# Kernel tuning notes

Measured on AMD Instinct MI355X. Metric: run time of the kernel, lower is better.

## Reference

```python
import jax, jax.numpy as jnp
import numpy as np

N = 100000
E = 1600000
D_IN = 128
D_HID = 128
D_OUT = 16


def setup_inputs() -> dict:
    key = jax.random.key(0)
    ks = jax.random.split(key, 10)
    x = jax.random.normal(ks[0], (N, D_IN), dtype=jnp.float32)
    edge_index = jax.random.randint(ks[1], (2, E), 0, N, dtype=jnp.int32)
    s = 1.0 / np.sqrt(D_IN)
    sh = 1.0 / np.sqrt(D_HID)
    W1l = jax.random.uniform(ks[2], (D_HID, D_IN), jnp.float32, -s, s)
    b1l = jax.random.uniform(ks[3], (D_HID,), jnp.float32, -s, s)
    W1r = jax.random.uniform(ks[4], (D_HID, D_IN), jnp.float32, -s, s)
    W2l = jax.random.uniform(ks[5], (D_HID, D_HID), jnp.float32, -sh, sh)
    b2l = jax.random.uniform(ks[6], (D_HID,), jnp.float32, -sh, sh)
    W2r = jax.random.uniform(ks[7], (D_HID, D_HID), jnp.float32, -sh, sh)
    Wc = jax.random.uniform(ks[8], (D_OUT, D_HID), jnp.float32, -sh, sh)
    bc = jax.random.uniform(ks[9], (D_OUT,), jnp.float32, -sh, sh)
    return {"x": x, "edge_index": edge_index, "W1l": W1l, "b1l": b1l, "W1r": W1r,
            "W2l": W2l, "b2l": b2l, "W2r": W2r, "Wc": Wc, "bc": bc}


def _sage_conv(x, src, dst, Wl, bl, Wr):
    # PyG SAGEConv (mean aggr): out_i = Wl @ mean_{j in N(i)} x_j + bl + Wr @ x_i
    n = x.shape[0]
    msg = x[src]                                             # [E, d] gather
    summed = jax.ops.segment_sum(msg, dst, num_segments=n)   # [N, d] scatter-add
    cnt = jax.ops.segment_sum(jnp.ones((src.shape[0],), x.dtype), dst, num_segments=n)
    agg = summed / jnp.maximum(cnt, 1.0)[:, None]            # mean; isolated nodes -> 0
    return agg @ Wl.T + bl + x @ Wr.T


def reference(x, edge_index, W1l, b1l, W1r, W2l, b2l, W2r, Wc, bc):
    src, dst = edge_index[0], edge_index[1]
    h = jax.nn.relu(_sage_conv(x, src, dst, W1l, b1l, W1r))
    # dropout p=0.5 is identity at inference (training=False)
    z = _sage_conv(h, src, dst, W2l, b2l, W2r)
    return z @ Wc.T + bc
```

## Files before the change

kernel.cpp:

```cpp
#include <hip/hip_runtime.h>

#define BSHIFT 9
#define BCAP   13312
#define CHUNK  8192

typedef __bf16 bf16x8 __attribute__((ext_vector_type(8)));
typedef float  f32x4  __attribute__((ext_vector_type(4)));
typedef float  f32x2  __attribute__((ext_vector_type(2)));

__device__ __forceinline__ unsigned short f2b(float f) {
  unsigned u = __float_as_uint(f);
  return (unsigned short)((u + 0x7fffu + ((u >> 16) & 1u)) >> 16);
}
__device__ __forceinline__ float b2f_lo(unsigned u) {
  return __uint_as_float(u << 16);
}
__device__ __forceinline__ float b2f_hi(unsigned u) {
  return __uint_as_float(u & 0xffff0000u);
}

__global__ __launch_bounds__(256) void k_front(
    const int* __restrict__ ei, int E, int* __restrict__ bcnt,
    unsigned* __restrict__ edg,
    const float* __restrict__ x, unsigned short* __restrict__ xb,
    unsigned* __restrict__ xq, int ngroups,
    const float* __restrict__ W1l, const float* __restrict__ W1r,
    unsigned short* __restrict__ Wb,
    const float* __restrict__ Wc, const float* __restrict__ bc,
    const float* __restrict__ W2l, const float* __restrict__ W2r,
    const float* __restrict__ b2, unsigned short* __restrict__ Mb,
    float* __restrict__ bias2,
    unsigned short* __restrict__ Pnb, int ZR, int nbin, int ncast) {
  __shared__ int lh[256], lbase[256], lcur[256];
  __shared__ int ldst[CHUNK];
  const int b = blockIdx.x;
  const int t = threadIdx.x;
  if (b < nbin) {
    lh[t] = 0; lcur[t] = 0;
    __syncthreads();
    const int e0 = b * CHUNK;
    const int n = min(E - e0, CHUNK);
    const int* __restrict__ src = ei;
    const int* __restrict__ dst = ei + E;
    for (int j = t; j < n; j += 256) {
      int d = dst[e0 + j];
      ldst[j] = d;
      atomicAdd(&lh[((unsigned)d) >> BSHIFT], 1);
    }
    __syncthreads();
    if (lh[t]) lbase[t] = atomicAdd(&bcnt[t], lh[t]);
    __syncthreads();
    for (int j = t; j < n; j += 256) {
      int d = ldst[j];
      unsigned s = (unsigned)src[e0 + j];
      int bk = ((unsigned)d) >> BSHIFT;
      int p = lbase[bk] + atomicAdd(&lcur[bk], 1);
      if (p < BCAP) edg[(size_t)bk * BCAP + p] = ((unsigned)(d & 511) << 17) | s;
    }
  } else if (b < nbin + ncast) {
    int g = (b - nbin) * 256 + t;
    if (g < ngroups) {
      float4 v = ((const float4*)x)[g];
      ushort4 o;
      o.x = f2b(v.x); o.y = f2b(v.y); o.z = f2b(v.z); o.w = f2b(v.w);
      ((ushort4*)xb)[g] = o;
      int q8 = __builtin_amdgcn_cvt_pk_fp8_f32(v.x, v.y, 0, false);
      q8 = __builtin_amdgcn_cvt_pk_fp8_f32(v.z, v.w, q8, true);
      xq[g] = (unsigned)q8;
    }
  } else {
    int bb = b - nbin - ncast;
    if (bb < 128) {
      int idx = bb * 256 + t;
      int col = idx >> 8, k = idx & 255;
      float v = (k < 128) ? W1l[col * 128 + k] : W1r[col * 128 + (k - 128)];
      Wb[col * 256 + k] = f2b(v);
    } else if (bb < 144) {
      int mb = bb - 128;
      int mat = mb >> 3;
      const float* W2 = mat ? W2r : W2l;
      int o = (mb & 7) * 2 + (t >> 7);
      int k = t & 127;
      float s = 0.f;
      for (int j = 0; j < 128; ++j) s = fmaf(Wc[o * 128 + j], W2[j * 128 + k], s);
      Mb[(size_t)(mat * 16 + o) * 128 + k] = f2b(s);
      if (mb == 0 && t < 16) {
        float sb = bc[t];
        for (int j = 0; j < 128; ++j) sb = fmaf(Wc[t * 128 + j], b2[j], sb);
        bias2[t] = sb;
      }
    } else {
      if (t < 64) ((unsigned*)(xb + (size_t)ZR * 128))[t] = 0;
      if (t < 32) xq[(size_t)ZR * 32 + t] = 0;
      if (t < 8)  ((unsigned*)(Pnb + (size_t)ZR * 16))[t] = 0;
    }
  }
}

__global__ __launch_bounds__(256) void k_build(
    const unsigned* __restrict__ edg, const int* __restrict__ bcnt,
    int* __restrict__ eidx, int* __restrict__ rowstart, int* __restrict__ cnt,
    int N, int ZR) {
  __shared__ int lsrc[BCAP];
  __shared__ int lcnt[512], lstart[512], lcur[512];
  __shared__ int wsum[4];
  const int b = blockIdx.x;
  const int t = threadIdx.x;
  const int node0 = b << BSHIFT;
  const int nb = min(512, N - node0);
  const int ecount = min(bcnt[b], BCAP);
  const unsigned* __restrict__ ed = edg + (size_t)b * BCAP;
  lcnt[2 * t] = 0; lcnt[2 * t + 1] = 0;
  for (int j = t; j < BCAP; j += 256) lsrc[j] = ZR;
  __syncthreads();
  for (int j = t; j < ecount; j += 256)
    atomicAdd(&lcnt[ed[j] >> 17], 1);
  __syncthreads();
  {
    int a0 = lcnt[2 * t], a1 = lcnt[2 * t + 1];
    int p0 = (a0 + 15) & ~15, p1 = (a1 + 15) & ~15;
    int s = p0 + p1, incl = s;
    int lane = t & 63, wv = t >> 6;
#pragma unroll
    for (int off = 1; off < 64; off <<= 1) {
      int v = __shfl_up(incl, off, 64);
      if (lane >= off) incl += v;
    }
    if (lane == 63) wsum[wv] = incl;
    __syncthreads();
    int woff = 0;
    for (int i = 0; i < wv; ++i) woff += wsum[i];
    int excl = woff + incl - s;
    lstart[2 * t] = excl;          lcur[2 * t] = excl;
    lstart[2 * t + 1] = excl + p0; lcur[2 * t + 1] = excl + p0;
  }
  __syncthreads();
  for (int j = t; j < ecount; j += 256) {
    unsigned e = ed[j];
    int p = atomicAdd(&lcur[e >> 17], 1);
    lsrc[p] = (int)(e & 0x1FFFFu);
  }
  __syncthreads();
  const int ebase = b * BCAP;
  int ecountp = min(wsum[0] + wsum[1] + wsum[2] + wsum[3], BCAP);
  for (int j = t; j < ecountp; j += 256) eidx[ebase + j] = lsrc[j];
  for (int i = t; i < nb; i += 256) {
    rowstart[node0 + i] = ebase + lstart[i];
    cnt[node0 + i] = lcnt[i];
  }
}

__global__ __launch_bounds__(256) void k_agg1(
    const int* __restrict__ eidx, const int* __restrict__ rowstart,
    const int* __restrict__ cnt,
    const unsigned* __restrict__ xq, unsigned short* __restrict__ aggb, int N) {
  int w = (blockIdx.x * 256 + threadIdx.x) >> 6;
  int lane = threadIdx.x & 63;
  if (w >= N) return;
  const int sub = lane >> 4;
  const int li = lane & 15;
  int deg = cnt[w];
  const int* el = eidx + rowstart[w];
  f32x2 acc[4];
#pragma unroll
  for (int j = 0; j < 4; ++j) acc[j] = (f32x2){0.f, 0.f};

  for (int e = 0; e < deg; e += 16) {
    int4 q = *(const int4*)(el + e + sub * 4);
    uint2 v0 = *(const uint2*)(xq + (size_t)q.x * 32 + li * 2);
    uint2 v1 = *(const uint2*)(xq + (size_t)q.y * 32 + li * 2);
    uint2 v2 = *(const uint2*)(xq + (size_t)q.z * 32 + li * 2);
    uint2 v3 = *(const uint2*)(xq + (size_t)q.w * 32 + li * 2);
#define ADD8(v)                                                      \
    acc[0] += __builtin_amdgcn_cvt_pk_f32_fp8(v.x, false);           \
    acc[1] += __builtin_amdgcn_cvt_pk_f32_fp8(v.x, true);            \
    acc[2] += __builtin_amdgcn_cvt_pk_f32_fp8(v.y, false);           \
    acc[3] += __builtin_amdgcn_cvt_pk_f32_fp8(v.y, true);
    ADD8(v0) ADD8(v1) ADD8(v2) ADD8(v3)
#undef ADD8
  }
#pragma unroll
  for (int j = 0; j < 4; ++j) {
    acc[j].x += __shfl_xor(acc[j].x, 16, 64);
    acc[j].y += __shfl_xor(acc[j].y, 16, 64);
    acc[j].x += __shfl_xor(acc[j].x, 32, 64);
    acc[j].y += __shfl_xor(acc[j].y, 32, 64);
  }
  if (sub == 0) {
    float sc = 1.0f / (float)max(deg, 1);
    uint2 o;
    uint4 o4;
    o4.x = (unsigned)f2b(acc[0].x * sc) | ((unsigned)f2b(acc[0].y * sc) << 16);
    o4.y = (unsigned)f2b(acc[1].x * sc) | ((unsigned)f2b(acc[1].y * sc) << 16);
    o4.z = (unsigned)f2b(acc[2].x * sc) | ((unsigned)f2b(acc[2].y * sc) << 16);
    o4.w = (unsigned)f2b(acc[3].x * sc) | ((unsigned)f2b(acc[3].y * sc) << 16);
    *(uint4*)(aggb + (size_t)w * 128 + li * 8) = o4;
    (void)o;
  }
}

__global__ __launch_bounds__(256) void k_gemm1_mfma(
    const unsigned short* __restrict__ aggb, const unsigned short* __restrict__ xb,
    const unsigned short* __restrict__ Wb, const float* __restrict__ b1,
    const unsigned short* __restrict__ Mb,
    unsigned short* __restrict__ Pnb, float* __restrict__ Ps, int N) {
  __shared__ union {
    struct { unsigned short A[128 * 40]; unsigned short W[128 * 40]; } s;
    unsigned short H[128 * 136];
  } sm;
  const int t = threadIdx.x;
  const int w = t >> 6;
  const int lane = t & 63;
  const int q = lane >> 4;
  const int l16 = lane & 15;
  const int row0 = blockIdx.x * 128;

  f32x4 acc[2][8];
#pragma unroll
  for (int rt = 0; rt < 2; ++rt)
#pragma unroll
    for (int ct = 0; ct < 8; ++ct) acc[rt][ct] = (f32x4){0.f, 0.f, 0.f, 0.f};

  for (int kc = 0; kc < 8; ++kc) {
    const unsigned short* Asrc = (kc < 4) ? aggb : xb;
    const int koff = (kc & 3) * 32;
#pragma unroll
    for (int i = 0; i < 2; ++i) {
      int idx = t + i * 256;
      int row = idx >> 2, c4 = idx & 3;
      int gr = row0 + row; if (gr >= N) gr = N - 1;
      uint4 v = *(const uint4*)(Asrc + (size_t)gr * 128 + koff + c4 * 8);
      *(uint4*)(sm.s.A + row * 40 + c4 * 8) = v;
    }
#pragma unroll
    for (int i = 0; i < 2; ++i) {
      int idx = t + i * 256;
      int col = idx >> 2, c4 = idx & 3;
      uint4 v = *(const uint4*)(Wb + col * 256 + kc * 32 + c4 * 8);
      *(uint4*)(sm.s.W + col * 40 + c4 * 8) = v;
    }
    __syncthreads();
    bf16x8 afr[2];
#pragma unroll
    for (int rt = 0; rt < 2; ++rt)
      afr[rt] = *(const bf16x8*)(sm.s.A + (w * 32 + rt * 16 + l16) * 40 + q * 8);
    bf16x8 bfr[8];
#pragma unroll
    for (int ct = 0; ct < 8; ++ct)
      bfr[ct] = *(const bf16x8*)(sm.s.W + (ct * 16 + l16) * 40 + q * 8);
#pragma unroll
    for (int rt = 0; rt < 2; ++rt)
#pragma unroll
      for (int ct = 0; ct < 8; ++ct)
        acc[rt][ct] = __builtin_amdgcn_mfma_f32_16x16x32_bf16(
            afr[rt], bfr[ct], acc[rt][ct], 0, 0, 0);
    __syncthreads();
  }

  float bv[8];
#pragma unroll
  for (int ct = 0; ct < 8; ++ct) bv[ct] = b1[ct * 16 + l16];
#pragma unroll
  for (int rt = 0; rt < 2; ++rt) {
    int rl = w * 32 + rt * 16 + q * 4;
#pragma unroll
    for (int reg = 0; reg < 4; ++reg) {
#pragma unroll
      for (int ct = 0; ct < 8; ++ct) {
        float v = acc[rt][ct][reg] + bv[ct];
        sm.H[(rl + reg) * 136 + ct * 16 + l16] = f2b(v > 0.f ? v : 0.f);
      }
    }
  }
  __syncthreads();

  f32x4 acc2[2][2];
#pragma unroll
  for (int rt = 0; rt < 2; ++rt)
#pragma unroll
    for (int ct = 0; ct < 2; ++ct) acc2[rt][ct] = (f32x4){0.f, 0.f, 0.f, 0.f};
#pragma unroll
  for (int ks = 0; ks < 4; ++ks) {
    bf16x8 a2[2], b2v[2];
#pragma unroll
    for (int rt = 0; rt < 2; ++rt)
      a2[rt] = *(const bf16x8*)(sm.H + (w * 32 + rt * 16 + l16) * 136 + ks * 32 + q * 8);
#pragma unroll
    for (int ct = 0; ct < 2; ++ct)
      b2v[ct] = *(const bf16x8*)(Mb + (size_t)(ct * 16 + l16) * 128 + ks * 32 + q * 8);
#pragma unroll
    for (int rt = 0; rt < 2; ++rt)
#pragma unroll
      for (int ct = 0; ct < 2; ++ct)
        acc2[rt][ct] = __builtin_amdgcn_mfma_f32_16x16x32_bf16(
            a2[rt], b2v[ct], acc2[rt][ct], 0, 0, 0);
  }
#pragma unroll
  for (int rt = 0; rt < 2; ++rt) {
    int rbase = row0 + w * 32 + rt * 16 + q * 4;
#pragma unroll
    for (int reg = 0; reg < 4; ++reg) {
      int r = rbase + reg;
      Pnb[(size_t)r * 16 + l16] = f2b(acc2[rt][0][reg]);
      Ps[(size_t)r * 16 + l16] = acc2[rt][1][reg];
    }
  }
}

__global__ __launch_bounds__(256) void k_agg2_out(
    const int* __restrict__ eidx, const int* __restrict__ rowstart,
    const int* __restrict__ cnt,
    const unsigned short* __restrict__ Pnb, const float* __restrict__ Ps,
    const float* __restrict__ bias2, float* __restrict__ out, int N) {
  int i = (blockIdx.x * 256 + threadIdx.x) >> 6;
  int lane = threadIdx.x & 63;
  if (i >= N) return;
  const int sub = lane >> 2;
  const int li = lane & 3;
  int deg = cnt[i];
  const int* el = eidx + rowstart[i];
  f32x2 a0 = (f32x2){0.f, 0.f}, a1 = (f32x2){0.f, 0.f};
  for (int e = 0; e < deg; e += 16) {
    int idx = el[e + sub];
    uint2 v = *(const uint2*)(Pnb + (size_t)idx * 16 + li * 4);
    a0 += (f32x2){b2f_lo(v.x), b2f_hi(v.x)};
    a1 += (f32x2){b2f_lo(v.y), b2f_hi(v.y)};
  }
#pragma unroll
  for (int m = 4; m <= 32; m <<= 1) {
    a0.x += __shfl_xor(a0.x, m, 64);
    a0.y += __shfl_xor(a0.y, m, 64);
    a1.x += __shfl_xor(a1.x, m, 64);
    a1.y += __shfl_xor(a1.y, m, 64);
  }
  if (sub == 0) {
    float sc = 1.0f / (float)max(deg, 1);
    float4 self = *(const float4*)(Ps + (size_t)i * 16 + li * 4);
    float4 b = *(const float4*)(bias2 + li * 4);
    float4 o;
    o.x = a0.x * sc + self.x + b.x;
    o.y = a0.y * sc + self.y + b.y;
    o.z = a1.x * sc + self.z + b.z;
    o.w = a1.y * sc + self.w + b.w;
    *(float4*)(out + (size_t)i * 16 + li * 4) = o;
  }
}

extern "C" void kernel_launch(void* const* d_in, const int* in_sizes, int n_in,
                              void* d_out, int out_size, void* d_ws, size_t ws_size,
                              hipStream_t stream) {
  const float* x   = (const float*)d_in[0];
  const int*   ei  = (const int*)d_in[1];
  const float* W1l = (const float*)d_in[2];
  const float* b1l = (const float*)d_in[3];
  const float* W1r = (const float*)d_in[4];
  const float* W2l = (const float*)d_in[5];
  const float* b2l = (const float*)d_in[6];
  const float* W2r = (const float*)d_in[7];
  const float* Wc  = (const float*)d_in[8];
  const float* bc  = (const float*)d_in[9];
  float* out = (float*)d_out;

  const int N     = in_sizes[0] / 128;
  const int E     = in_sizes[1] / 2;
  const int Np    = ((N + 127) / 128) * 128;
  const int NBUCK = (N + 511) >> BSHIFT;
  const int ZR    = Np;
  const int NBIN  = (E + CHUNK - 1) / CHUNK;
  const int NCAST = (N * 32 + 255) / 256;

  char* ws = (char*)d_ws;
  size_t off = 0;
  auto alloc = [&](size_t bytes) {
    void* p = ws + off;
    off = (off + bytes + 255) & ~(size_t)255;
    return p;
  };
  int*            cnt      = (int*)           alloc((size_t)N * 4);
  int*            rowstart = (int*)           alloc((size_t)N * 4);
  int*            bcnt     = (int*)           alloc(256 * 4);
  unsigned*       edg      = (unsigned*)      alloc((size_t)NBUCK * BCAP * 4);
  int*            eidx     = (int*)           alloc((size_t)NBUCK * BCAP * 4);
  unsigned short* xb       = (unsigned short*)alloc((size_t)(Np + 1) * 128 * 2);
  unsigned*       xq       = (unsigned*)      alloc((size_t)(Np + 1) * 32 * 4);
  unsigned short* aggb     = (unsigned short*)alloc((size_t)Np * 128 * 2);
  unsigned short* Wb       = (unsigned short*)alloc((size_t)128 * 256 * 2);
  unsigned short* Mb       = (unsigned short*)alloc((size_t)32 * 128 * 2);
  unsigned short* Pnb      = (unsigned short*)alloc((size_t)(Np + 1) * 16 * 2);
  float*          Ps       = (float*)         alloc((size_t)Np * 16 * 4);
  float*          bias2    = (float*)         alloc(16 * 4);
  (void)ws_size; (void)n_in; (void)out_size;

  hipMemsetAsync(bcnt, 0, 256 * 4, stream);
  k_front<<<NBIN + NCAST + 145, 256, 0, stream>>>(
      ei, E, bcnt, edg, x, xb, xq, N * 32,
      W1l, W1r, Wb, Wc, bc, W2l, W2r, b2l, Mb, bias2, Pnb, ZR, NBIN, NCAST);
  k_build<<<NBUCK, 256, 0, stream>>>(edg, bcnt, eidx, rowstart, cnt, N, ZR);
  k_agg1<<<(N + 3) / 4, 256, 0, stream>>>(eidx, rowstart, cnt, xq, aggb, N);
  k_gemm1_mfma<<<Np / 128, 256, 0, stream>>>(aggb, xb, Wb, b1l, Mb, Pnb, Ps, N);
  k_agg2_out<<<(N + 3) / 4, 256, 0, stream>>>(eidx, rowstart, cnt, Pnb, Ps, bias2, out, N);
}
```

Baseline: 259.1 us.

## Replace bucketed CSR build with global histogram, scan, and atomic scatter

The CSR construction changes. Previously edges were binned into fixed-capacity per-512-node buckets and then sorted in shared memory. Now it computes a global per-node degree histogram with global atomics, runs a per-block padded scan that takes its global offset from an atomic counter, and scatters source indices with per-node atomic cursors. Row start and count are packed into one int2 so each aggregation needs a single load. This removes the BCAP overflow truncation and the intermediate bucket buffer, but it adds an extra kernel, heavy global atomics on random addresses, and an N-sized memset. Blocks now claim their offsets in arbitrary order, so node rows lose contiguous locality in eidx.

```diff
diff --git a/kernel.cpp b/kernel.cpp
--- a/kernel.cpp
+++ b/kernel.cpp
@@ -1,8 +1,4 @@
 #include <hip/hip_runtime.h>
-
-#define BSHIFT 9
-#define BCAP   13312
-#define CHUNK  8192
 
 typedef __bf16 bf16x8 __attribute__((ext_vector_type(8)));
 typedef float  f32x4  __attribute__((ext_vector_type(4)));
@@ -20,8 +16,7 @@
 }
 
 __global__ __launch_bounds__(256) void k_front(
-    const int* __restrict__ ei, int E, int* __restrict__ bcnt,
-    unsigned* __restrict__ edg,
+    const int* __restrict__ ei, int E, int* __restrict__ cnt,
     const float* __restrict__ x, unsigned short* __restrict__ xb,
     unsigned* __restrict__ xq, int ngroups,
     const float* __restrict__ W1l, const float* __restrict__ W1r,
@@ -30,35 +25,16 @@
     const float* __restrict__ W2l, const float* __restrict__ W2r,
     const float* __restrict__ b2, unsigned short* __restrict__ Mb,
     float* __restrict__ bias2,
-    unsigned short* __restrict__ Pnb, int ZR, int nbin, int ncast) {
-  __shared__ int lh[256], lbase[256], lcur[256];
-  __shared__ int ldst[CHUNK];
+    unsigned short* __restrict__ Pnb, int ZR, int nhist, int ncast) {
   const int b = blockIdx.x;
   const int t = threadIdx.x;
-  if (b < nbin) {
-    lh[t] = 0; lcur[t] = 0;
-    __syncthreads();
-    const int e0 = b * CHUNK;
-    const int n = min(E - e0, CHUNK);
-    const int* __restrict__ src = ei;
+  if (b < nhist) {
     const int* __restrict__ dst = ei + E;
-    for (int j = t; j < n; j += 256) {
-      int d = dst[e0 + j];
-      ldst[j] = d;
-      atomicAdd(&lh[((unsigned)d) >> BSHIFT], 1);
-    }
-    __syncthreads();
-    if (lh[t]) lbase[t] = atomicAdd(&bcnt[t], lh[t]);
-    __syncthreads();
-    for (int j = t; j < n; j += 256) {
-      int d = ldst[j];
-      unsigned s = (unsigned)src[e0 + j];
-      int bk = ((unsigned)d) >> BSHIFT;
-      int p = lbase[bk] + atomicAdd(&lcur[bk], 1);
-      if (p < BCAP) edg[(size_t)bk * BCAP + p] = ((unsigned)(d & 511) << 17) | s;
-    }
-  } else if (b < nbin + ncast) {
-    int g = (b - nbin) * 256 + t;
+    const int stride = nhist * 256;
+    for (int j = b * 256 + t; j < E; j += stride)
+      atomicAdd(&cnt[dst[j]], 1);
+  } else if (b < nhist + ncast) {
+    int g = (b - nhist) * 256 + t;
     if (g < ngroups) {
       float4 v = ((const float4*)x)[g];
       ushort4 o;
@@ -69,7 +45,7 @@
       xq[g] = (unsigned)q8;
     }
   } else {
-    int bb = b - nbin - ncast;
+    int bb = b - nhist - ncast;
     if (bb < 128) {
       int idx = bb * 256 + t;
       int col = idx >> 8, k = idx & 255;
@@ -97,70 +73,73 @@
   }
 }
 
-__global__ __launch_bounds__(256) void k_build(
-    const unsigned* __restrict__ edg, const int* __restrict__ bcnt,
-    int* __restrict__ eidx, int* __restrict__ rowstart, int* __restrict__ cnt,
-    int N, int ZR) {
-  __shared__ int lsrc[BCAP];
-  __shared__ int lcnt[512], lstart[512], lcur[512];
+__global__ __launch_bounds__(256) void k_scan(
+    const int* __restrict__ cnt, int* __restrict__ rowcnt,
+    int* __restrict__ cur, int* __restrict__ eidx,
+    int* __restrict__ gptr, int N, int ZR) {
   __shared__ int wsum[4];
+  __shared__ int sbase;
   const int b = blockIdx.x;
   const int t = threadIdx.x;
-  const int node0 = b << BSHIFT;
-  const int nb = min(512, N - node0);
-  const int ecount = min(bcnt[b], BCAP);
-  const unsigned* __restrict__ ed = edg + (size_t)b * BCAP;
-  lcnt[2 * t] = 0; lcnt[2 * t + 1] = 0;
-  for (int j = t; j < BCAP; j += 256) lsrc[j] = ZR;
+  const int node0 = b * 512;
+  const int i0 = node0 + 2 * t;
+  const int i1 = i0 + 1;
+  int c0 = (i0 < N) ? cnt[i0] : 0;
+  int c1 = (i1 < N) ? cnt[i1] : 0;
+  int p0 = (c0 + 15) & ~15;
+  int p1 = (c1 + 15) & ~15;
+  int s = p0 + p1, incl = s;
+  int lane = t & 63, wv = t >> 6;
+#pragma unroll
+  for (int off = 1; off < 64; off <<= 1) {
+    int v = __shfl_up(incl, off, 64);
+    if (lane >= off) incl += v;
+  }
+  if (lane == 63) wsum[wv] = incl;
   __syncthreads();
-  for (int j = t; j < ecount; j += 256)
-    atomicAdd(&lcnt[ed[j] >> 17], 1);
+  int woff = 0;
+  for (int k = 0; k < wv; ++k) woff += wsum[k];
+  if (t == 0) {
+    int tot = wsum[0] + wsum[1] + wsum[2] + wsum[3];
+    sbase = atomicAdd(gptr, tot);
+  }
   __syncthreads();
-  {
-    int a0 = lcnt[2 * t], a1 = lcnt[2 * t + 1];
-    int p0 = (a0 + 15) & ~15, p1 = (a1 + 15) & ~15;
-    int s = p0 + p1, incl = s;
-    int lane = t & 63, wv = t >> 6;
-#pragma unroll
-    for (int off = 1; off < 64; off <<= 1) {
-      int v = __shfl_up(incl, off, 64);
-      if (lane >= off) incl += v;
-    }
-    if (lane == 63) wsum[wv] = incl;
-    __syncthreads();
-    int woff = 0;
-    for (int i = 0; i < wv; ++i) woff += wsum[i];
-    int excl = woff + incl - s;
-    lstart[2 * t] = excl;          lcur[2 * t] = excl;
-    lstart[2 * t + 1] = excl + p0; lcur[2 * t + 1] = excl + p0;
-  }
-  __syncthreads();
-  for (int j = t; j < ecount; j += 256) {
-    unsigned e = ed[j];
-    int p = atomicAdd(&lcur[e >> 17], 1);
-    lsrc[p] = (int)(e & 0x1FFFFu);
-  }
-  __syncthreads();
-  const int ebase = b * BCAP;
-  int ecountp = min(wsum[0] + wsum[1] + wsum[2] + wsum[3], BCAP);
-  for (int j = t; j < ecountp; j += 256) eidx[ebase + j] = lsrc[j];
-  for (int i = t; i < nb; i += 256) {
-    rowstart[node0 + i] = ebase + lstart[i];
-    cnt[node0 + i] = lcnt[i];
+  const int e0 = sbase + woff + incl - s;
+  const int e1 = e0 + p0;
+  if (i0 < N) {
+    rowcnt[2 * i0] = e0; rowcnt[2 * i0 + 1] = c0; cur[i0] = e0;
+    for (int j = c0; j < p0; ++j) eidx[e0 + j] = ZR;
+  }
+  if (i1 < N) {
+    rowcnt[2 * i1] = e1; rowcnt[2 * i1 + 1] = c1; cur[i1] = e1;
+    for (int j = c1; j < p1; ++j) eidx[e1 + j] = ZR;
+  }
+}
+
+__global__ __launch_bounds__(256) void k_scatter(
+    const int* __restrict__ ei, int E,
+    int* __restrict__ cur, int* __restrict__ eidx) {
+  const int* __restrict__ src = ei;
+  const int* __restrict__ dst = ei + E;
+  const int stride = gridDim.x * 256;
+  for (int j = blockIdx.x * 256 + threadIdx.x; j < E; j += stride) {
+    int d = dst[j];
+    int p = atomicAdd(&cur[d], 1);
+    eidx[p] = src[j];
   }
 }
 
 __global__ __launch_bounds__(256) void k_agg1(
-    const int* __restrict__ eidx, const int* __restrict__ rowstart,
-    const int* __restrict__ cnt,
+    const int* __restrict__ eidx, const int* __restrict__ rowcnt,
     const unsigned* __restrict__ xq, unsigned short* __restrict__ aggb, int N) {
   int w = (blockIdx.x * 256 + threadIdx.x) >> 6;
   int lane = threadIdx.x & 63;
   if (w >= N) return;
   const int sub = lane >> 4;
   const int li = lane & 15;
-  int deg = cnt[w];
-  const int* el = eidx + rowstart[w];
+  int2 rc = *(const int2*)(rowcnt + 2 * (size_t)w);
+  int deg = rc.y;
+  const int* el = eidx + rc.x;
   f32x2 acc[4];
 #pragma unroll
   for (int j = 0; j < 4; ++j) acc[j] = (f32x2){0.f, 0.f};
@@ -188,14 +167,12 @@
   }
   if (sub == 0) {
     float sc = 1.0f / (float)max(deg, 1);
-    uint2 o;
     uint4 o4;
     o4.x = (unsigned)f2b(acc[0].x * sc) | ((unsigned)f2b(acc[0].y * sc) << 16);
     o4.y = (unsigned)f2b(acc[1].x * sc) | ((unsigned)f2b(acc[1].y * sc) << 16);
     o4.z = (unsigned)f2b(acc[2].x * sc) | ((unsigned)f2b(acc[2].y * sc) << 16);
     o4.w = (unsigned)f2b(acc[3].x * sc) | ((unsigned)f2b(acc[3].y * sc) << 16);
     *(uint4*)(aggb + (size_t)w * 128 + li * 8) = o4;
-    (void)o;
   }
 }
 
@@ -308,8 +285,7 @@
 }
 
 __global__ __launch_bounds__(256) void k_agg2_out(
-    const int* __restrict__ eidx, const int* __restrict__ rowstart,
-    const int* __restrict__ cnt,
+    const int* __restrict__ eidx, const int* __restrict__ rowcnt,
     const unsigned short* __restrict__ Pnb, const float* __restrict__ Ps,
     const float* __restrict__ bias2, float* __restrict__ out, int N) {
   int i = (blockIdx.x * 256 + threadIdx.x) >> 6;
@@ -317,8 +293,9 @@
   if (i >= N) return;
   const int sub = lane >> 2;
   const int li = lane & 3;
-  int deg = cnt[i];
-  const int* el = eidx + rowstart[i];
+  int2 rc = *(const int2*)(rowcnt + 2 * (size_t)i);
+  int deg = rc.y;
+  const int* el = eidx + rc.x;
   f32x2 a0 = (f32x2){0.f, 0.f}, a1 = (f32x2){0.f, 0.f};
   for (int e = 0; e < deg; e += 16) {
     int idx = el[e + sub];
@@ -364,9 +341,8 @@
   const int N     = in_sizes[0] / 128;
   const int E     = in_sizes[1] / 2;
   const int Np    = ((N + 127) / 128) * 128;
-  const int NBUCK = (N + 511) >> BSHIFT;
   const int ZR    = Np;
-  const int NBIN  = (E + CHUNK - 1) / CHUNK;
+  const int NHIST = 1024;
   const int NCAST = (N * 32 + 255) / 256;
 
   char* ws = (char*)d_ws;
@@ -377,10 +353,10 @@
     return p;
   };
   int*            cnt      = (int*)           alloc((size_t)N * 4);
-  int*            rowstart = (int*)           alloc((size_t)N * 4);
-  int*            bcnt     = (int*)           alloc(256 * 4);
-  unsigned*       edg      = (unsigned*)      alloc((size_t)NBUCK * BCAP * 4);
-  int*            eidx     = (int*)           alloc((size_t)NBUCK * BCAP * 4);
+  int*            rowcnt   = (int*)           alloc((size_t)N * 8);
+  int*            cur      = (int*)           alloc((size_t)N * 4);
+  int*            gptr     = (int*)           alloc(256);
+  int*            eidx     = (int*)           alloc(((size_t)E + 16 * (size_t)N) * 4);
   unsigned short* xb       = (unsigned short*)alloc((size_t)(Np + 1) * 128 * 2);
   unsigned*       xq       = (unsigned*)      alloc((size_t)(Np + 1) * 32 * 4);
   unsigned short* aggb     = (unsigned short*)alloc((size_t)Np * 128 * 2);
@@ -391,12 +367,14 @@
   float*          bias2    = (float*)         alloc(16 * 4);
   (void)ws_size; (void)n_in; (void)out_size;
 
-  hipMemsetAsync(bcnt, 0, 256 * 4, stream);
-  k_front<<<NBIN + NCAST + 145, 256, 0, stream>>>(
-      ei, E, bcnt, edg, x, xb, xq, N * 32,
-      W1l, W1r, Wb, Wc, bc, W2l, W2r, b2l, Mb, bias2, Pnb, ZR, NBIN, NCAST);
-  k_build<<<NBUCK, 256, 0, stream>>>(edg, bcnt, eidx, rowstart, cnt, N, ZR);
-  k_agg1<<<(N + 3) / 4, 256, 0, stream>>>(eidx, rowstart, cnt, xq, aggb, N);
+  hipMemsetAsync(cnt, 0, (size_t)N * 4, stream);
+  hipMemsetAsync(gptr, 0, 4, stream);
+  k_front<<<NHIST + NCAST + 145, 256, 0, stream>>>(
+      ei, E, cnt, x, xb, xq, N * 32,
+      W1l, W1r, Wb, Wc, bc, W2l, W2r, b2l, Mb, bias2, Pnb, ZR, NHIST, NCAST);
+  k_scan<<<(N + 511) / 512, 256, 0, stream>>>(cnt, rowcnt, cur, eidx, gptr, N, ZR);
+  k_scatter<<<2048, 256, 0, stream>>>(ei, E, cur, eidx);
+  k_agg1<<<(N + 3) / 4, 256, 0, stream>>>(eidx, rowcnt, xq, aggb, N);
   k_gemm1_mfma<<<Np / 128, 256, 0, stream>>>(aggb, xb, Wb, b1l, Mb, Pnb, Ps, N);
-  k_agg2_out<<<(N + 3) / 4, 256, 0, stream>>>(eidx, rowstart, cnt, Pnb, Ps, bias2, out, N);
-}
+  k_agg2_out<<<(N + 3) / 4, 256, 0, stream>>>(eidx, rowcnt, Pnb, Ps, bias2, out, N);
+}
```

New measurement: 417.1 us. 1.61x slower.
